# Performance work log

Measured on AMD Instinct MI355X. Metric: run time of the kernel, lower is better.

## Reference

```python
import jax, jax.numpy as jnp
import numpy as np


def _box_filter(img):
    # img: [B,1,H,W]; 5x5 uniform kernel, padding=4 -> output [B,1,H+4,W+4]
    k = jnp.full((1, 1, 5, 5), 1.0 / 25.0, dtype=img.dtype)
    return jax.lax.conv_general_dilated(
        img, k, window_strides=(1, 1), padding=((4, 4), (4, 4)),
        dimension_numbers=('NCHW', 'OIHW', 'NCHW'))


def setup_inputs() -> dict:
    key = jax.random.key(0)
    k1, k2 = jax.random.split(key)
    x = jax.random.normal(k1, (64, 1, 512, 512), dtype=jnp.float32)
    y = jax.random.normal(k2, (64, 1, 512, 512), dtype=jnp.float32)
    return {"x": x, "y": y}


def reference(x, y):
    diff = _box_filter(x) - _box_filter(y)
    # faithful to torch.mean(torch.sqrt(diff * diff)) (== mean(|diff|))
    return jnp.mean(jnp.sqrt(diff * diff))
```

## Files before the change

kernel.cpp:

```cpp
#include <hip/hip_runtime.h>


#define IMG_W 512
#define IMG_H 512
#define OUT_W 516
#define OUT_H 516
#define R     17
#define SPI   31
#define NT    256
#define WAVES (NT / 64)
#define NSTRIPS (64 * SPI)
#define NBLK  (NSTRIPS / WAVES)
#define NPART 64
#define NROWS 21

typedef float v4f __attribute__((ext_vector_type(4)));

#define LOADCHUNK(base, nr)                                               \
    __builtin_amdgcn_sched_barrier(0);                                    \
    _Pragma("unroll")                                                     \
    for (int q = 0; q < (nr); ++q) {                                      \
        const int rc = min(max(i0 - 4 + (base) + q, 0), IMG_H - 1);       \
        const float* xr = xb + (size_t)rc * IMG_W;                        \
        xa[q] = *(const v4f*)(xr); xc[q] = *(const v4f*)(xr + 4);         \
    }                                                                     \
    _Pragma("unroll")                                                     \
    for (int q = 0; q < (nr); ++q) {                                      \
        const int rc = min(max(i0 - 4 + (base) + q, 0), IMG_H - 1);       \
        const float* yr = yb + (size_t)rc * IMG_W;                        \
        ya[q] = *(const v4f*)(yr); yc[q] = *(const v4f*)(yr + 4);         \
    }                                                                     \
    __builtin_amdgcn_sched_barrier(0);

__global__ __launch_bounds__(NT, 2) void box_loss_kernel(
    const float* __restrict__ x, const float* __restrict__ y,
    float* __restrict__ partial)
{
    const int t    = threadIdx.x;
    const int lane = t & 63;
    const int wid  = t >> 6;

    const int bid  = blockIdx.x;
    const int swz  = (bid & 7) * (NBLK / 8) + (bid >> 3);

    const int strip = swz * WAVES + wid;
    const int b  = strip / SPI;
    const int s  = strip - b * SPI;
    const int i0 = s * R;
    const int c0 = lane * 8;

    const float* xb = x + (size_t)b * (IMG_W * IMG_H) + c0;
    const float* yb = y + (size_t)b * (IMG_W * IMG_H) + c0;

    v4f xa[5], xc[5], ya[5], yc[5];

    float ring[5][8];
    float v[8];
    #pragma unroll
    for (int j = 0; j < 8; ++j) { v[j] = 0.f; ring[4][j] = 0.f; }

    float acc = 0.f;

    #pragma unroll
    for (int k = 0; k < NROWS; ++k) {
        if (k == 0)  { LOADCHUNK(0, 4);  }
        if (k == 4)  { LOADCHUNK(4, 4);  }
        if (k == 8)  { LOADCHUNK(8, 4);  }
        if (k == 12) { LOADCHUNK(12, 4); }
        if (k == 16) { LOADCHUNK(16, 5); }
        const int mI = (k < 4) ? k : (k < 8) ? (k - 4) : (k < 12) ? (k - 8)
                     : (k < 16) ? (k - 12) : (k - 16);
        const int r = i0 - 4 + k;
        const float m = (r >= 0 && r < IMG_H) ? 1.f : 0.f;

        float d[8];
        d[0] = (xa[mI].x - ya[mI].x) * m; d[1] = (xa[mI].y - ya[mI].y) * m;
        d[2] = (xa[mI].z - ya[mI].z) * m; d[3] = (xa[mI].w - ya[mI].w) * m;
        d[4] = (xc[mI].x - yc[mI].x) * m; d[5] = (xc[mI].y - yc[mI].y) * m;
        d[6] = (xc[mI].z - yc[mI].z) * m; d[7] = (xc[mI].w - yc[mI].w) * m;

        if (k < 4) {
            #pragma unroll
            for (int j = 0; j < 8; ++j) { ring[k][j] = d[j]; v[j] += d[j]; }
        } else {
            const int i = i0 + (k - 4);
            const int slot = k % 5;
            #pragma unroll
            for (int j = 0; j < 8; ++j) {
                v[j] += d[j] - ring[slot][j];
                ring[slot][j] = d[j];
            }

            float h0 = __shfl_up(v[4], 1, 64);
            float h1 = __shfl_up(v[5], 1, 64);
            float h2 = __shfl_up(v[6], 1, 64);
            float h3 = __shfl_up(v[7], 1, 64);
            if (lane == 0) { h0 = 0.f; h1 = 0.f; h2 = 0.f; h3 = 0.f; }

            const float s0 = h0 + h1 + h2 + h3 + v[0];
            const float s1 = s0 + v[1] - h0;
            const float s2 = s1 + v[2] - h1;
            const float s3 = s2 + v[3] - h2;
            const float s4 = s3 + v[4] - h3;
            const float s5 = s4 + v[5] - v[0];
            const float s6 = s5 + v[6] - v[1];
            const float s7 = s6 + v[7] - v[2];

            const float rowmask = (i < OUT_H) ? 1.f : 0.f;
            acc += rowmask * (fabsf(s0) + fabsf(s1) + fabsf(s2) + fabsf(s3)
                            + fabsf(s4) + fabsf(s5) + fabsf(s6) + fabsf(s7));

            const float em = (lane == 63) ? rowmask : 0.f;
            const float e0 = v[4] + v[5] + v[6] + v[7];
            const float e1 = v[5] + v[6] + v[7];
            const float e2 = v[6] + v[7];
            const float e3 = v[7];
            acc += em * (fabsf(e0) + fabsf(e1) + fabsf(e2) + fabsf(e3));
        }
    }

    #pragma unroll
    for (int off = 32; off > 0; off >>= 1)
        acc += __shfl_down(acc, off, 64);
    if (lane == 0)
        atomicAdd(partial + (strip & (NPART - 1)), acc);
}

__global__ void finalize_kernel(const float* __restrict__ partial,
                                float* __restrict__ out)
{
    float s = 0.f;
    #pragma unroll
    for (int k = 0; k < NPART; ++k) s += partial[k];
    out[0] = s * (1.0f / (25.0f * 64.0f * 516.0f * 516.0f));
}

extern "C" void kernel_launch(void* const* d_in, const int* in_sizes, int n_in,
                              void* d_out, int out_size, void* d_ws, size_t ws_size,
                              hipStream_t stream) {
    const float* x = (const float*)d_in[0];
    const float* y = (const float*)d_in[1];
    float* out = (float*)d_out;
    float* ws  = (float*)d_ws;

    hipMemsetAsync(ws, 0, NPART * sizeof(float), stream);

    dim3 grid(NBLK);
    box_loss_kernel<<<grid, NT, 0, stream>>>(x, y, ws);
    finalize_kernel<<<1, 1, 0, stream>>>(ws, out);
}
```

Before: 149.1 us.

## Split each row strip across two waves with LDS halo handoff

```diff
diff --git a/kernel.cpp b/kernel.cpp
--- a/kernel.cpp
+++ b/kernel.cpp
@@ -8,29 +8,12 @@
 #define R     17
 #define SPI   31
 #define NT    256
-#define WAVES (NT / 64)
-#define NSTRIPS (64 * SPI)
-#define NBLK  (NSTRIPS / WAVES)
+#define NGRP  (64 * SPI)
+#define NBLK  (NGRP / 2)
 #define NPART 64
 #define NROWS 21
 
 typedef float v4f __attribute__((ext_vector_type(4)));
-
-#define LOADCHUNK(base, nr)                                               \
-    __builtin_amdgcn_sched_barrier(0);                                    \
-    _Pragma("unroll")                                                     \
-    for (int q = 0; q < (nr); ++q) {                                      \
-        const int rc = min(max(i0 - 4 + (base) + q, 0), IMG_H - 1);       \
-        const float* xr = xb + (size_t)rc * IMG_W;                        \
-        xa[q] = *(const v4f*)(xr); xc[q] = *(const v4f*)(xr + 4);         \
-    }                                                                     \
-    _Pragma("unroll")                                                     \
-    for (int q = 0; q < (nr); ++q) {                                      \
-        const int rc = min(max(i0 - 4 + (base) + q, 0), IMG_H - 1);       \
-        const float* yr = yb + (size_t)rc * IMG_W;                        \
-        ya[q] = *(const v4f*)(yr); yc[q] = *(const v4f*)(yr + 4);         \
-    }                                                                     \
-    __builtin_amdgcn_sched_barrier(0);
 
 __global__ __launch_bounds__(NT, 2) void box_loss_kernel(
     const float* __restrict__ x, const float* __restrict__ y,
@@ -39,91 +22,118 @@
     const int t    = threadIdx.x;
     const int lane = t & 63;
     const int wid  = t >> 6;
+    const int pair = wid >> 1;
+    const int h    = wid & 1;
 
     const int bid  = blockIdx.x;
     const int swz  = (bid & 7) * (NBLK / 8) + (bid >> 3);
 
-    const int strip = swz * WAVES + wid;
-    const int b  = strip / SPI;
-    const int s  = strip - b * SPI;
+    const int g  = swz * 2 + pair;
+    const int b  = g / SPI;
+    const int s  = g - b * SPI;
     const int i0 = s * R;
-    const int c0 = lane * 8;
+    const int c0 = h * 256 + 4 * lane;
 
     const float* xb = x + (size_t)b * (IMG_W * IMG_H) + c0;
     const float* yb = y + (size_t)b * (IMG_W * IMG_H) + c0;
 
-    v4f xa[5], xc[5], ya[5], yc[5];
+    __shared__ float snap[2][2][8][4];
 
-    float ring[5][8];
-    float v[8];
+    v4f sx[8], sy[8];
+
+    float ring[5][4];
+    float v[4];
     #pragma unroll
-    for (int j = 0; j < 8; ++j) { v[j] = 0.f; ring[4][j] = 0.f; }
+    for (int j = 0; j < 4; ++j) { v[j] = 0.f; ring[4][j] = 0.f; }
 
     float acc = 0.f;
 
-    #pragma unroll
-    for (int k = 0; k < NROWS; ++k) {
-        if (k == 0)  { LOADCHUNK(0, 4);  }
-        if (k == 4)  { LOADCHUNK(4, 4);  }
-        if (k == 8)  { LOADCHUNK(8, 4);  }
-        if (k == 12) { LOADCHUNK(12, 4); }
-        if (k == 16) { LOADCHUNK(16, 5); }
-        const int mI = (k < 4) ? k : (k < 8) ? (k - 4) : (k < 12) ? (k - 8)
-                     : (k < 16) ? (k - 12) : (k - 16);
-        const int r = i0 - 4 + k;
-        const float m = (r >= 0 && r < IMG_H) ? 1.f : 0.f;
+#define STAGE(base, nr)                                                   \
+    __builtin_amdgcn_sched_barrier(0);                                    \
+    _Pragma("unroll")                                                     \
+    for (int q = 0; q < (nr); ++q) {                                      \
+        const int rc = min(max(i0 - 4 + (base) + q, 0), IMG_H - 1);       \
+        sx[q] = *(const v4f*)(xb + (size_t)rc * IMG_W);                   \
+    }                                                                     \
+    _Pragma("unroll")                                                     \
+    for (int q = 0; q < (nr); ++q) {                                      \
+        const int rc = min(max(i0 - 4 + (base) + q, 0), IMG_H - 1);       \
+        sy[q] = *(const v4f*)(yb + (size_t)rc * IMG_W);                   \
+    }                                                                     \
+    __builtin_amdgcn_sched_barrier(0);
 
-        float d[8];
-        d[0] = (xa[mI].x - ya[mI].x) * m; d[1] = (xa[mI].y - ya[mI].y) * m;
-        d[2] = (xa[mI].z - ya[mI].z) * m; d[3] = (xa[mI].w - ya[mI].w) * m;
-        d[4] = (xc[mI].x - yc[mI].x) * m; d[5] = (xc[mI].y - yc[mI].y) * m;
-        d[6] = (xc[mI].z - yc[mI].z) * m; d[7] = (xc[mI].w - yc[mI].w) * m;
+#define CONSUME(base, nr, buf, isLeft)                                    \
+    _Pragma("unroll")                                                     \
+    for (int q = 0; q < (nr); ++q) {                                      \
+        const int k = (base) + q;                \
+        const int r = i0 - 4 + k;                                         \
+        const float m = (r >= 0 && r < IMG_H) ? 1.f : 0.f;                \
+        float d[4];                                                       \
+        d[0] = (sx[q].x - sy[q].x) * m; d[1] = (sx[q].y - sy[q].y) * m;   \
+        d[2] = (sx[q].z - sy[q].z) * m; d[3] = (sx[q].w - sy[q].w) * m;   \
+        if (k < 4) {                                                      \
+            _Pragma("unroll")                                             \
+            for (int j = 0; j < 4; ++j) { ring[k][j] = d[j]; v[j] += d[j]; } \
+        } else {                                                          \
+            const int slot = k % 5;                                       \
+            _Pragma("unroll")                                             \
+            for (int j = 0; j < 4; ++j) {                                 \
+                v[j] += d[j] - ring[slot][j]; ring[slot][j] = d[j];       \
+            }                                                             \
+            float h0 = __shfl_up(v[0], 1, 64);                            \
+            float h1 = __shfl_up(v[1], 1, 64);                            \
+            float h2 = __shfl_up(v[2], 1, 64);                            \
+            float h3 = __shfl_up(v[3], 1, 64);                            \
+            if (isLeft) {                                                 \
+                if (lane == 0) { h0 = 0.f; h1 = 0.f; h2 = 0.f; h3 = 0.f; }\
+                if (lane == 63) {                                         \
+                    snap[pair][buf][q][0] = v[0];                         \
+                    snap[pair][buf][q][1] = v[1];                         \
+                    snap[pair][buf][q][2] = v[2];                         \
+                    snap[pair][buf][q][3] = v[3];                         \
+                }                                                         \
+            } else {                                                      \
+                if (lane == 0) {                                          \
+                    h0 = snap[pair][buf][q][0];                           \
+                    h1 = snap[pair][buf][q][1];                           \
+                    h2 = snap[pair][buf][q][2];                           \
+                    h3 = snap[pair][buf][q][3];                           \
+                }                                                         \
+            }                                                             \
+            const float s0 = h0 + h1 + h2 + h3 + v[0];                    \
+            const float s1 = s0 - h0 + v[1];                              \
+            const float s2 = s1 - h1 + v[2];                              \
+            const float s3 = s2 - h2 + v[3];                              \
+            const int i = i0 + (k - 4);                                   \
+            const float rowmask = (i < OUT_H) ? 1.f : 0.f;                \
+            acc += rowmask * (fabsf(s0) + fabsf(s1)                       \
+                            + fabsf(s2) + fabsf(s3));                     \
+            if (!(isLeft) && lane == 63) {                                \
+                const float e0 = v[0] + v[1] + v[2] + v[3];               \
+                const float e1 = v[1] + v[2] + v[3];                      \
+                const float e2 = v[2] + v[3];                             \
+                const float e3 = v[3];                                    \
+                acc += rowmask * (fabsf(e0) + fabsf(e1)                   \
+                                + fabsf(e2) + fabsf(e3));                 \
+            }                                                             \
+        }                                                                 \
+    }
 
-        if (k < 4) {
-            #pragma unroll
-            for (int j = 0; j < 8; ++j) { ring[k][j] = d[j]; v[j] += d[j]; }
-        } else {
-            const int i = i0 + (k - 4);
-            const int slot = k % 5;
-            #pragma unroll
-            for (int j = 0; j < 8; ++j) {
-                v[j] += d[j] - ring[slot][j];
-                ring[slot][j] = d[j];
-            }
+#define CHUNK(base, nr, cidx)                                             \
+    STAGE(base, nr)                                                       \
+    if (h == 0) { CONSUME(base, nr, (cidx) & 1, true) }                   \
+    __syncthreads();                                                      \
+    if (h == 1) { CONSUME(base, nr, (cidx) & 1, false) }
 
-            float h0 = __shfl_up(v[4], 1, 64);
-            float h1 = __shfl_up(v[5], 1, 64);
-            float h2 = __shfl_up(v[6], 1, 64);
-            float h3 = __shfl_up(v[7], 1, 64);
-            if (lane == 0) { h0 = 0.f; h1 = 0.f; h2 = 0.f; h3 = 0.f; }
-
-            const float s0 = h0 + h1 + h2 + h3 + v[0];
-            const float s1 = s0 + v[1] - h0;
-            const float s2 = s1 + v[2] - h1;
-            const float s3 = s2 + v[3] - h2;
-            const float s4 = s3 + v[4] - h3;
-            const float s5 = s4 + v[5] - v[0];
-            const float s6 = s5 + v[6] - v[1];
-            const float s7 = s6 + v[7] - v[2];
-
-            const float rowmask = (i < OUT_H) ? 1.f : 0.f;
-            acc += rowmask * (fabsf(s0) + fabsf(s1) + fabsf(s2) + fabsf(s3)
-                            + fabsf(s4) + fabsf(s5) + fabsf(s6) + fabsf(s7));
-
-            const float em = (lane == 63) ? rowmask : 0.f;
-            const float e0 = v[4] + v[5] + v[6] + v[7];
-            const float e1 = v[5] + v[6] + v[7];
-            const float e2 = v[6] + v[7];
-            const float e3 = v[7];
-            acc += em * (fabsf(e0) + fabsf(e1) + fabsf(e2) + fabsf(e3));
-        }
-    }
+    CHUNK(0, 8, 0)
+    CHUNK(8, 8, 1)
+    CHUNK(16, 5, 2)
 
     #pragma unroll
     for (int off = 32; off > 0; off >>= 1)
         acc += __shfl_down(acc, off, 64);
     if (lane == 0)
-        atomicAdd(partial + (strip & (NPART - 1)), acc);
+        atomicAdd(partial + ((g * 2 + h) & (NPART - 1)), acc);
 }
 
 __global__ void finalize_kernel(const float* __restrict__ partial,
```

New measurement: 152.9 us. 2.6% more time.
